# Kernel optimization log

Hardware: AMD Instinct MI355X
Metric: run time of the kernel (lower is better)

The kernel has to match this reference:

```python
import math
import jax, jax.numpy as jnp
from jax import lax
import numpy as np

SQRT2 = 1.4142135623730951
LR_MLP = 0.01


def _blur_kernel():
    k = jnp.array([1., 3., 3., 1.], dtype=jnp.float32)
    k = k[:, None] * k[None, :]
    return k / jnp.sum(k)


def upfirdn2d(x, kernel, up, pad0, pad1):
    # x: (B,C,H,W). Matches torch upfirdn2d_native (flip kernel, zero-upsample, pad, correlate).
    B, C, H, W = x.shape
    x = x.reshape(B * C, 1, H, W)
    k = jnp.flip(kernel, (0, 1))[None, None]
    p1 = pad1 + (up - 1)  # lax lhs_dilation omits trailing zeros of upfirdn upsampling
    out = lax.conv_general_dilated(x, k, (1, 1), ((pad0, p1), (pad0, p1)), lhs_dilation=(up, up))
    return out.reshape(B, C, out.shape[-2], out.shape[-1])


def pixel_norm(x, eps=1e-6):
    norm = jnp.sqrt(jnp.sum(x * x, axis=1, keepdims=True))
    norm = norm / math.sqrt(x.shape[1])
    return x / (norm + eps)


def fused_act(x, b):
    return jax.nn.leaky_relu(x + b[None, :, None, None], 0.2) * SQRT2


def mod_conv(x, w, sw, sb, lat, demodulate, up):
    # w: (Cout,Cin,kh,kw); sw: (Cin, style_ch) equalized-lr linear; lat: (B, style_ch)
    Cout, Cin, kh, kw = w.shape
    s = lat @ (sw.T * (1.0 / math.sqrt(sw.shape[1]))) + sb  # (B, Cin), bias_init=1
    wm = (w * (1.0 / math.sqrt(Cin * kh * kw)))[None] * s[:, None, :, None, None]
    if demodulate:
        d = lax.rsqrt(jnp.sum(wm * wm, axis=(2, 3, 4)) + 1e-8)
        wm = wm * d[:, :, None, None, None]
    if up:
        # per-sample conv_transpose(stride=2, pad=0) == dilated conv with flipped kernel
        def f(xi, wi):
            return lax.conv_general_dilated(xi[None], jnp.flip(wi, (2, 3)), (1, 1),
                                            ((kh - 1, kh - 1), (kw - 1, kw - 1)),
                                            lhs_dilation=(2, 2))[0]
        out = jax.vmap(f)(x, wm)
        out = upfirdn2d(out, _blur_kernel() * 4.0, 1, 1, 1)  # Blur pad=(1,1), k*factor^2
    else:
        pad = kh // 2
        def f(xi, wi):
            return lax.conv_general_dilated(xi[None], wi, (1, 1), ((pad, pad), (pad, pad)))[0]
        out = jax.vmap(f)(x, wm)
    return out


def style_mapping(z, W, Bv):
    x = pixel_norm(z)
    sc = 1.0 / math.sqrt(W.shape[-1])
    for i in range(W.shape[0]):
        x = jax.nn.leaky_relu(x @ (W[i].T * sc) + Bv[i] * LR_MLP, 0.2) * SQRT2
    return x


def setup_inputs() -> dict:
    key = jax.random.key(0)
    ks = jax.random.split(key, 32)
    B = 32
    inp = {
        'z': jax.random.normal(ks[0], (B, 512), jnp.float32),
        'mlp_w': jax.random.normal(ks[1], (8, 512, 512), jnp.float32),
        'mlp_b': jax.random.normal(ks[2], (8, 512), jnp.float32),
        'const_input': jax.random.normal(ks[3], (1, 512, 4, 4), jnp.float32),
        'conv_w': jax.random.normal(ks[4], (9, 512, 512, 3, 3), jnp.float32),
        'conv_style_w': jax.random.normal(ks[5], (9, 512, 512), jnp.float32),
        'conv_style_b': jnp.ones((9, 512), jnp.float32),
        'noise_w': jax.random.normal(ks[6], (9,), jnp.float32),
        'act_bias': jnp.zeros((9, 512), jnp.float32),
        'torgb_w': jax.random.normal(ks[7], (5, 3, 512, 1, 1), jnp.float32),
        'torgb_style_w': jax.random.normal(ks[8], (5, 512, 512), jnp.float32),
        'torgb_style_b': jnp.ones((5, 512), jnp.float32),
        'torgb_bias': jnp.zeros((5, 3), jnp.float32),
    }
    sizes = [4, 8, 8, 16, 16, 32, 32, 64, 64]
    for i, s in enumerate(sizes):
        inp[f'noise{i}'] = jax.random.normal(ks[10 + i], (B, 1, s, s), jnp.float32)
    return inp


def reference(z, mlp_w, mlp_b, const_input, conv_w, conv_style_w, conv_style_b,
              noise_w, act_bias, torgb_w, torgb_style_w, torgb_style_b, torgb_bias,
              noise0, noise1, noise2, noise3, noise4, noise5, noise6, noise7, noise8):
    noises = [noise0, noise1, noise2, noise3, noise4, noise5, noise6, noise7, noise8]
    w = style_mapping(z, mlp_w, mlp_b)  # single style injection -> same w for all layers
    B = z.shape[0]
    x = jnp.tile(const_input, (B, 1, 1, 1))

    def sconv(x, i, up):
        out = mod_conv(x, conv_w[i], conv_style_w[i], conv_style_b[i], w, True, up)
        out = out + noise_w[i] * noises[i]
        return fused_act(out, act_bias[i])

    def trgb(x, j):
        out = mod_conv(x, torgb_w[j], torgb_style_w[j], torgb_style_b[j], w, False, False)
        return out + torgb_bias[j][None, :, None, None]

    x = sconv(x, 0, False)
    skip = trgb(x, 0)
    bk = _blur_kernel() * 4.0
    for r in range(4):  # resolutions 8,16,32,64
        x = sconv(x, 1 + 2 * r, True)
        x = sconv(x, 2 + 2 * r, False)
        skip = trgb(x, r + 1) + upfirdn2d(skip, bk, 2, 2, 1)  # UpsampleUpFIRDn pad=(2,1)
    return skip  # (B,3,64,64)
```

## Files before the change

kernel.cpp:

```cpp
#include <hip/hip_runtime.h>
#include <hip/hip_bf16.h>
#include <cstdio>
#include <math.h>


static constexpr int NB = 32;
static constexpr float SQRT2F      = 1.41421356237309515f;
static constexpr float INV_SQRT512 = 0.04419417382415922f;
static constexpr float INV_SQRT4608= 0.014731391274719742f;

typedef __hip_bfloat16 bf16;
typedef __attribute__((ext_vector_type(8))) short bf16x8;
typedef __attribute__((ext_vector_type(4))) float f32x4;

#define GLOAD_LDS16(src, dst) __builtin_amdgcn_global_load_lds( \
    (const __attribute__((address_space(1))) void*)(src), \
    (__attribute__((address_space(3))) void*)(dst), 16, 0, 0)

__device__ __forceinline__ float lrelu_s2(float v){ return (v > 0.f ? v : 0.2f*v) * SQRT2F; }
__device__ __forceinline__ float bf_lo(unsigned u){ unsigned v = u << 16; return __builtin_bit_cast(float, v); }
__device__ __forceinline__ float bf_hi(unsigned u){ unsigned v = u & 0xffff0000u; return __builtin_bit_cast(float, v); }
__device__ __forceinline__ unsigned packbf2(float a, float b){
  bf16 ha = __float2bfloat16(a), hb = __float2bfloat16(b);
  unsigned short ra = __builtin_bit_cast(unsigned short, ha);
  unsigned short rb = __builtin_bit_cast(unsigned short, hb);
  return (unsigned)ra | ((unsigned)rb << 16);
}

__global__ void k_mapping(const float* __restrict__ z, const float* __restrict__ mlp_w,
                          const float* __restrict__ mlp_b, float* __restrict__ wlat){
  __shared__ float xb[512], yb[512], red[256];
  int b = blockIdx.x, t = threadIdx.x;
  float z0 = z[b*512 + t], z1 = z[b*512 + t + 256];
  red[t] = z0*z0 + z1*z1;
  __syncthreads();
  for(int s = 128; s > 0; s >>= 1){ if(t < s) red[t] += red[t+s]; __syncthreads(); }
  float norm = sqrtf(red[0]) * INV_SQRT512;
  float inv = 1.f / (norm + 1e-6f);
  xb[t] = z0*inv; xb[t+256] = z1*inv;
  __syncthreads();
  for(int l = 0; l < 8; l++){
    const float* Wl = mlp_w + (size_t)l*512*512;
    const float* bl = mlp_b + l*512;
    for(int oo = 0; oo < 2; oo++){
      int o = t + oo*256;
      const float4* wr = (const float4*)(Wl + (size_t)o*512);
      float acc = 0.f;
      #pragma unroll 4
      for(int k = 0; k < 128; k++){
        float4 w4 = wr[k];
        acc += w4.x*xb[4*k] + w4.y*xb[4*k+1] + w4.z*xb[4*k+2] + w4.w*xb[4*k+3];
      }
      yb[o] = lrelu_s2(acc*INV_SQRT512 + bl[o]*0.01f);
    }
    __syncthreads();
    xb[t] = yb[t]; xb[t+256] = yb[t+256];
    __syncthreads();
  }
  wlat[b*512+t] = xb[t]; wlat[b*512+t+256] = xb[t+256];
}

__global__ void k_styles(const float* __restrict__ wlat,
                         const float* __restrict__ csw, const float* __restrict__ csb,
                         const float* __restrict__ tsw, const float* __restrict__ tsb,
                         float* __restrict__ s_conv, float* __restrict__ s_trgb){
  int gid = blockIdx.x*256 + threadIdx.x;
  int l = gid >> 14;
  int b = (gid >> 9) & 31;
  int i = gid & 511;
  const float* row; float bias, wsc;
  if(l < 9){ row = csw + ((size_t)l*512 + i)*512; bias = csb[l*512+i]; wsc = INV_SQRT4608; }
  else     { int lt = l-9; row = tsw + ((size_t)lt*512 + i)*512; bias = tsb[lt*512+i]; wsc = INV_SQRT512; }
  const float4* r4 = (const float4*)row;
  const float4* w4 = (const float4*)(wlat + b*512);
  float acc = 0.f;
  #pragma unroll 4
  for(int k = 0; k < 128; k++){
    float4 a = w4[k], c = r4[k];
    acc += a.x*c.x + a.y*c.y + a.z*c.z + a.w*c.w;
  }
  float s = (acc*INV_SQRT512 + bias) * wsc;
  if(l < 9) s_conv[((size_t)l*32 + b)*512 + i] = s;
  else      s_trgb[((size_t)(l-9)*32 + b)*512 + i] = s;
}

__global__ void k_prep(const float* __restrict__ cw, float* __restrict__ wsq,
                       bf16* __restrict__ wB){
  int gid = blockIdx.x*256 + threadIdx.x;
  const float* p = cw + (size_t)gid*9;
  int l = gid >> 18;
  int oi = gid & 0x3ffff;
  float v[9]; float a = 0.f;
  #pragma unroll
  for(int t = 0; t < 9; t++){ v[t] = p[t]; a += v[t]*v[t]; }
  wsq[gid] = a;
  #pragma unroll
  for(int tap = 0; tap < 9; tap++)
    wB[((size_t)(l*9 + tap) << 18) + oi] = __float2bfloat16(v[tap]);
}

__global__ void k_demod(const float* __restrict__ s_conv, const float* __restrict__ wsq,
                        float* __restrict__ d_conv){
  __shared__ float s2[512];
  int l = blockIdx.x/32, b = blockIdx.x%32, t = threadIdx.x;
  size_t base = ((size_t)l*32 + b)*512;
  float v0 = s_conv[base + t], v1 = s_conv[base + t + 256];
  s2[t] = v0*v0; s2[t+256] = v1*v1;
  __syncthreads();
  for(int oo = 0; oo < 2; oo++){
    int o = t + oo*256;
    const float4* wr = (const float4*)(wsq + ((size_t)l*512 + o)*512);
    float acc = 0.f;
    #pragma unroll 4
    for(int k = 0; k < 128; k++){
      float4 w = wr[k];
      acc += w.x*s2[4*k] + w.y*s2[4*k+1] + w.z*s2[4*k+2] + w.w*s2[4*k+3];
    }
    d_conv[base + o] = rsqrtf(acc + 1e-8f);
  }
}

__global__ void k_ratio(const float* __restrict__ s_conv, const float* __restrict__ s_trgb,
                        float* __restrict__ rat){
  int gid = blockIdx.x*256 + threadIdx.x;
  int lt = gid >> 14;
  if(lt >= 4){ rat[gid] = 1.0f; return; }
  int b = (gid >> 9) & 31;
  int i = gid & 511;
  int cl = 1 + 2*lt;
  float st = s_trgb[((size_t)lt*32 + b)*512 + i];
  float sc = s_conv[((size_t)cl*32 + b)*512 + i];
  rat[gid] = (sc != 0.f) ? st/sc : 0.f;
}

__global__ void k_init(const float* __restrict__ ci, const float* __restrict__ s_conv,
                       bf16* __restrict__ act){
  int gid = blockIdx.x*256 + threadIdx.x;
  int c = gid & 511; int px = (gid >> 9) & 15; int b = gid >> 13;
  act[gid] = __float2bfloat16(ci[c*16 + px] * s_conv[b*512 + c]);
}

template<bool UP>
__global__ __launch_bounds__(256, 2)
void k_conv(const bf16* __restrict__ act, const bf16* __restrict__ wL,
            const float* __restrict__ dL, const float* __restrict__ noise,
            const float* __restrict__ nw_ptr, const float* __restrict__ ab,
            const float* __restrict__ sN, bf16* __restrict__ outp,
            const bf16* __restrict__ zp, int Hin, int Mblocks){
  const int q8 = gridDim.x >> 3;
  const int swzb = (blockIdx.x & 7)*q8 + (blockIdx.x >> 3);
  const int nb = swzb & 3, mb = swzb >> 2;
  if(mb >= Mblocks) return;
  const int mbase = mb*128, nbase = nb*128;

  int py = 0, px = 0;
  int OHy, OHx;
  if(UP){
    int cls = blockIdx.z; py = cls >> 1; px = cls & 1;
    OHy = Hin + 1 - py; OHx = Hin + 1 - px;
  } else {
    OHy = Hin; OHx = Hin;
  }
  const int pixN = OHy*OHx;
  const int Mtot = NB*pixN;
  if(mbase >= Mtot) return;

  __shared__ short As[2][128*64];
  __shared__ short Bs[2][128*64];
  const int t = threadIdx.x;
  const int wid  = t >> 6;
  const int lane = t & 63;
  const int rloc = lane >> 3;
  const int slot = lane & 7;

  int swz[4]; int gbv[4], gYv[4], gXv[4]; bool mv[4];
  const bf16* bB[4];
  #pragma unroll
  for(int i = 0; i < 4; i++){
    int r = wid*32 + i*8 + rloc;
    swz[i] = slot ^ (r & 7);
    int m = mbase + r; mv[i] = (m < Mtot); int mm = mv[i] ? m : 0;
    gbv[i] = mm / pixN; int rem = mm % pixN; gYv[i] = rem / OHx; gXv[i] = rem % OHx;
    bB[i] = wL + ((size_t)(nbase + r) << 9) + swz[i]*8;
  }

  const int mrow0 = (wid >> 1)*64;
  const int ncol0 = (wid & 1)*64;
  const int lr = t & 15;
  const int ks = (t & 63) >> 4;
  const int lr7 = lr & 7;
  const int sw0 = (ks ^ lr7)*8;
  const int sw1 = ((4 + ks) ^ lr7)*8;

  f32x4 acc[4][4];
  #pragma unroll
  for(int i = 0; i < 4; i++)
    #pragma unroll
    for(int j = 0; j < 4; j++) acc[i][j] = (f32x4){0.f,0.f,0.f,0.f};

  int dyl[3], dxl[3], ndy, ndx;
  if(UP){
    if(py == 0){ dyl[0]=0; dyl[1]=2; ndy=2; } else { dyl[0]=1; ndy=1; }
    if(px == 0){ dxl[0]=0; dxl[1]=2; ndx=2; } else { dxl[0]=1; ndx=1; }
  } else {
    dyl[0]=0; dyl[1]=1; dyl[2]=2; ndy=3;
    dxl[0]=0; dxl[1]=1; dxl[2]=2; ndx=3;
  }
  const int TT = ndy*ndx;

  auto mkA = [&](int dy, int dx, const bf16** aA){
    #pragma unroll
    for(int i = 0; i < 4; i++){
      int yy, xx;
      if(UP){ yy = gYv[i] - ((dy - py) >> 1); xx = gXv[i] - ((dx - px) >> 1); }
      else  { yy = gYv[i] + dy - 1;           xx = gXv[i] + dx - 1; }
      bool ok = mv[i] && ((unsigned)yy < (unsigned)Hin) && ((unsigned)xx < (unsigned)Hin);
      aA[i] = ok ? (act + (((size_t)((gbv[i]*Hin + yy)*Hin + xx)) << 9) + swz[i]*8) : zp;
    }
  };
  auto issue = [&](const bf16** aA, int tapIdx, int c, int bb){
    #pragma unroll
    for(int i = 0; i < 4; i++)
      GLOAD_LDS16(aA[i] + c*64, &As[bb][(wid*32 + i*8)*64]);
    #pragma unroll
    for(int i = 0; i < 4; i++)
      GLOAD_LDS16(bB[i] + ((size_t)tapIdx << 18) + c*64, &Bs[bb][(wid*32 + i*8)*64]);
  };

  const bf16* aC[4]; const bf16* aN[4];
  int tapC = dyl[0]*3 + dxl[0], tapN = 0;
  mkA(dyl[0], dxl[0], aC);
  issue(aC, tapC, 0, 0);

  for(int tt = 0; tt < TT; tt++){
    const bool haveNextTap = (tt + 1 < TT);
    if(haveNextTap){
      int dyN = dyl[(tt+1)/ndx], dxN = dxl[(tt+1)%ndx];
      tapN = dyN*3 + dxN;
      mkA(dyN, dxN, aN);
    }
    #pragma unroll
    for(int c = 0; c < 8; c++){
      const int bb = c & 1;
      bool issued = true;
      if(c < 7)               issue(aC, tapC, c+1, bb^1);
      else if(haveNextTap)    issue(aN, tapN, 0,   bb^1);
      else                    issued = false;
      if(issued) asm volatile("s_waitcnt vmcnt(8)" ::: "memory");
      else       asm volatile("s_waitcnt vmcnt(0)" ::: "memory");
      __builtin_amdgcn_s_barrier();
      #pragma unroll
      for(int h = 0; h < 2; h++){
        const int swr = h ? sw1 : sw0;
        bf16x8 af[4], bfr[4];
        #pragma unroll
        for(int f = 0; f < 4; f++){
          af[f]  = *(const bf16x8*)&As[bb][(mrow0 + f*16 + lr)*64 + swr];
          bfr[f] = *(const bf16x8*)&Bs[bb][(ncol0 + f*16 + lr)*64 + swr];
        }
        __builtin_amdgcn_s_setprio(1);
        #pragma unroll
        for(int mf = 0; mf < 4; mf++)
          #pragma unroll
          for(int nf = 0; nf < 4; nf++)
            acc[mf][nf] = __builtin_amdgcn_mfma_f32_16x16x32_bf16(af[mf], bfr[nf], acc[mf][nf], 0, 0, 0);
        __builtin_amdgcn_s_setprio(0);
      }
      asm volatile("s_waitcnt lgkmcnt(0)" ::: "memory");
      __builtin_amdgcn_s_barrier();
    }
    if(haveNextTap){
      #pragma unroll
      for(int i = 0; i < 4; i++) aC[i] = aN[i];
      tapC = tapN;
    }
  }

  const float nwv = UP ? 0.f : *nw_ptr;
  const int U = 2*Hin + 1;
  #pragma unroll
  for(int mf = 0; mf < 4; mf++){
    #pragma unroll
    for(int r = 0; r < 4; r++){
      int me = mbase + mrow0 + mf*16 + ks*4 + r;
      if(me >= Mtot) continue;
      int b = me / pixN; int rem2 = me % pixN; int y = rem2 / OHx, x = rem2 % OHx;
      const float* drow = dL + b*512;
      bf16* orow;
      float nz = 0.f; const float* srow = nullptr;
      if(UP){
        orow = outp + (((size_t)((b*U + 2*y + py))*U + (2*x + px)) << 9);
      } else {
        nz = nwv * noise[(b*OHy + y)*OHx + x];
        srow = sN + b*512;
        orow = outp + ((size_t)me << 9);
      }
      #pragma unroll
      for(int nf = 0; nf < 4; nf++){
        int n = nbase + ncol0 + nf*16 + lr;
        float val = acc[mf][nf][r] * drow[n];
        if(!UP) val = lrelu_s2(val + nz + ab[n]) * srow[n];
        orow[n] = __float2bfloat16(val);
      }
    }
  }
}

__global__ void k_blurF(const bf16* __restrict__ u, const float* __restrict__ noise,
                        const float* __restrict__ nw_ptr, const float* __restrict__ ab,
                        const float* __restrict__ sN, bf16* __restrict__ act, int O){
  const int U = O + 1;
  __shared__ unsigned vrow[65*64];
  const int bid = blockIdx.x;
  const int cq = bid & 3;
  const int rowid = bid >> 2;
  const int Y = rowid % O; const int b = rowid / O;
  const int t = threadIdx.x;
  const int ch2 = t & 63;
  const int cg  = t >> 6;
  const float k1[4] = {0.25f, 0.75f, 0.75f, 0.25f};

  for(int it = 0; it < (65 + 3)/4; it++){
    int col = it*4 + cg;
    if(col < U){
      float a0 = 0.f, a1 = 0.f;
      #pragma unroll
      for(int ky = 0; ky < 4; ky++){
        int yy = Y + ky - 1; if(yy < 0 || yy >= U) continue;
        unsigned uv = *(const unsigned*)(u + (((size_t)(b*U + yy)*U + col) << 9) + cq*128 + ch2*2);
        a0 += k1[ky]*bf_lo(uv); a1 += k1[ky]*bf_hi(uv);
      }
      vrow[col*64 + ch2] = packbf2(a0, a1);
    }
  }
  __syncthreads();
  const float nwv = *nw_ptr;
  const float abA = ab[cq*128 + ch2*2], abB = ab[cq*128 + ch2*2 + 1];
  const float sA  = sN[b*512 + cq*128 + ch2*2], sB = sN[b*512 + cq*128 + ch2*2 + 1];
  for(int it = 0; it < (64 + 3)/4; it++){
    int X = it*4 + cg;
    if(X < O){
      float a0 = 0.f, a1 = 0.f;
      #pragma unroll
      for(int kx = 0; kx < 4; kx++){
        int xx = X + kx - 1; if(xx < 0 || xx >= U) continue;
        unsigned v = vrow[xx*64 + ch2];
        a0 += k1[kx]*bf_lo(v); a1 += k1[kx]*bf_hi(v);
      }
      float nz = nwv * noise[(b*O + Y)*O + X];
      unsigned pk = packbf2(lrelu_s2(a0 + nz + abA)*sA, lrelu_s2(a1 + nz + abB)*sB);
      *(unsigned*)(act + (((size_t)(b*O + Y)*O + X) << 9) + cq*128 + ch2*2) = pk;
    }
  }
}

__global__ void k_torgb(const bf16* __restrict__ act, const float* __restrict__ tw,
                        const float* __restrict__ ratL, const float* __restrict__ tbias,
                        float* __restrict__ dst, int H, int lt, int addflag){
  int wid = threadIdx.x >> 6, lane = threadIdx.x & 63;
  int pix = blockIdx.x*4 + wid;
  int npix = NB*H*H;
  if(pix >= npix) return;
  int b = pix/(H*H);
  const bf16* ap = act + ((size_t)pix << 9);
  const float* rp = ratL + (size_t)b*512;
  const float* w0 = tw + ((size_t)lt*3 + 0)*512;
  const float* w1 = tw + ((size_t)lt*3 + 1)*512;
  const float* w2 = tw + ((size_t)lt*3 + 2)*512;
  float a0 = 0.f, a1 = 0.f, a2 = 0.f;
  #pragma unroll
  for(int j = 0; j < 8; j++){
    int i = lane + j*64;
    float xs = __bfloat162float(ap[i])*rp[i];
    a0 += xs*w0[i]; a1 += xs*w1[i]; a2 += xs*w2[i];
  }
  for(int off = 32; off > 0; off >>= 1){
    a0 += __shfl_xor(a0, off);
    a1 += __shfl_xor(a1, off);
    a2 += __shfl_xor(a2, off);
  }
  if(lane == 0){
    int rem = pix % (H*H);
    size_t o0 = ((size_t)(b*3 + 0)*H*H) + rem;
    size_t o1 = ((size_t)(b*3 + 1)*H*H) + rem;
    size_t o2 = ((size_t)(b*3 + 2)*H*H) + rem;
    float b0 = tbias[lt*3+0], b1 = tbias[lt*3+1], b2 = tbias[lt*3+2];
    if(addflag){ dst[o0] += a0 + b0; dst[o1] += a1 + b1; dst[o2] += a2 + b2; }
    else       { dst[o0]  = a0 + b0; dst[o1]  = a1 + b1; dst[o2]  = a2 + b2; }
  }
}

__global__ void k_skipup(const float* __restrict__ sin, float* __restrict__ sout, int h){
  const int O = 2*h;
  int gid = blockIdx.x*256 + threadIdx.x;
  int total = NB*3*O*O;
  if(gid >= total) return;
  int X = gid % O; int Y = (gid/O) % O; int c = (gid/(O*O)) % 3; int b = gid/(3*O*O);
  const float k1[4] = {1.f, 3.f, 3.f, 1.f};
  float acc = 0.f;
  for(int ky = (Y & 1); ky < 4; ky += 2){
    int ty = Y + ky - 2;
    if(ty < 0) continue;
    int y = ty >> 1; if(y >= h) continue;
    for(int kx = (X & 1); kx < 4; kx += 2){
      int tx = X + kx - 2;
      if(tx < 0) continue;
      int x = tx >> 1; if(x >= h) continue;
      acc += k1[ky]*k1[kx]*(1.f/16.f) * sin[((size_t)(b*3 + c)*h + y)*h + x];
    }
  }
  sout[gid] = acc;
}

extern "C" void kernel_launch(void* const* d_in, const int* in_sizes, int n_in,
                              void* d_out, int out_size, void* d_ws, size_t ws_size,
                              hipStream_t stream){
  const float* z     = (const float*)d_in[0];
  const float* mlp_w = (const float*)d_in[1];
  const float* mlp_b = (const float*)d_in[2];
  const float* cinp  = (const float*)d_in[3];
  const float* conv_w= (const float*)d_in[4];
  const float* csw   = (const float*)d_in[5];
  const float* csb   = (const float*)d_in[6];
  const float* nwp   = (const float*)d_in[7];
  const float* abp   = (const float*)d_in[8];
  const float* tw    = (const float*)d_in[9];
  const float* tsw   = (const float*)d_in[10];
  const float* tsb   = (const float*)d_in[11];
  const float* tb    = (const float*)d_in[12];
  const float* noise[9];
  for(int i = 0; i < 9; i++) noise[i] = (const float*)d_in[13 + i];

  const size_t UMAX = (size_t)32*65*65*512;
  char* base = (char*)d_ws;
  size_t off = 0;
  bf16* buf0 = (bf16*)(base + off); off += UMAX*2;
  bf16* buf1 = (bf16*)(base + off); off += UMAX*2;
  bf16* wB   = (bf16*)(base + off); off += (size_t)9*9*512*512*2;
  float* wsq = (float*)(base + off); off += (size_t)9*512*512*4;
  float* wlat= (float*)(base + off); off += (size_t)32*512*4;
  float* sconv=(float*)(base + off); off += (size_t)9*32*512*4;
  float* dconv=(float*)(base + off); off += (size_t)9*32*512*4;
  float* strgb=(float*)(base + off); off += (size_t)5*32*512*4;
  float* rat  =(float*)(base + off); off += (size_t)5*32*512*4;
  float* skipA=(float*)(base + off); off += (size_t)32*3*64*64*4;
  float* skipB=(float*)(base + off); off += (size_t)32*3*64*64*4;
  bf16* zpage=(bf16*)(base + off); off += 2048;
  if(ws_size < off){
    fprintf(stderr, "kernel_launch: ws too small (%zu < %zu)\n", ws_size, off);
    return;
  }
  float* out = (float*)d_out;

  hipMemsetAsync(zpage, 0, 2048, stream);
  k_mapping<<<32, 256, 0, stream>>>(z, mlp_w, mlp_b, wlat);
  k_styles <<<896, 256, 0, stream>>>(wlat, csw, csb, tsw, tsb, sconv, strgb);
  k_prep   <<<9216, 256, 0, stream>>>(conv_w, wsq, wB);
  k_demod  <<<288, 256, 0, stream>>>(sconv, wsq, dconv);
  k_ratio  <<<320, 256, 0, stream>>>(sconv, strgb, rat);
  k_init   <<<1024, 256, 0, stream>>>(cinp, sconv, buf0);

  auto conv_noup = [&](const bf16* in, bf16* o, int H, int layer, const float* sN){
    int M = 32*H*H; int Mb = (M + 127)/128;
    int Gx = ((Mb*4 + 7)/8)*8;
    k_conv<false><<<dim3(Gx,1,1), 256, 0, stream>>>(in, wB + ((size_t)layer*9 << 18),
        dconv + (size_t)layer*NB*512, noise[layer], nwp + layer, abp + layer*512, sN, o, zpage, H, Mb);
  };
  auto conv_up = [&](const bf16* in, bf16* o, int Hin, int layer){
    int Mmax = 32*(Hin+1)*(Hin+1); int Mb = (Mmax + 127)/128;
    int Gx = ((Mb*4 + 7)/8)*8;
    k_conv<true><<<dim3(Gx,1,4), 256, 0, stream>>>(in, wB + ((size_t)layer*9 << 18),
        dconv + (size_t)layer*NB*512, nullptr, nullptr, nullptr, nullptr, o, zpage, Hin, Mb);
  };
  auto blur = [&](const bf16* u, bf16* o, int O, int layer, const float* sN){
    int blocks = 32*O*4;
    k_blurF<<<blocks, 256, 0, stream>>>(u, noise[layer], nwp + layer,
        abp + layer*512, sN, o, O);
  };
  auto torgb = [&](const bf16* act, float* dst, int H, int lt, int add){
    int npix = 32*H*H;
    k_torgb<<<(npix + 3)/4, 256, 0, stream>>>(act, tw, rat + (size_t)lt*NB*512, tb, dst, H, lt, add);
  };
  auto skipup = [&](const float* sin, float* sout, int h){
    int total = 32*3*(2*h)*(2*h);
    k_skipup<<<(total + 255)/256, 256, 0, stream>>>(sin, sout, h);
  };

  const float* S = sconv;
  const float* sT4 = strgb + (size_t)4*NB*512;

  conv_noup(buf0, buf1, 4, 0, S + (size_t)1*NB*512);
  torgb(buf1, skipA, 4, 0, 0);

  conv_up(buf1, buf0, 4, 1);
  blur(buf0, buf1, 8, 1, S + (size_t)2*NB*512);
  conv_noup(buf1, buf0, 8, 2, S + (size_t)3*NB*512);
  skipup(skipA, skipB, 4);
  torgb(buf0, skipB, 8, 1, 1);

  conv_up(buf0, buf1, 8, 3);
  blur(buf1, buf0, 16, 3, S + (size_t)4*NB*512);
  conv_noup(buf0, buf1, 16, 4, S + (size_t)5*NB*512);
  skipup(skipB, skipA, 8);
  torgb(buf1, skipA, 16, 2, 1);

  conv_up(buf1, buf0, 16, 5);
  blur(buf0, buf1, 32, 5, S + (size_t)6*NB*512);
  conv_noup(buf1, buf0, 32, 6, S + (size_t)7*NB*512);
  skipup(skipA, skipB, 16);
  torgb(buf0, skipB, 32, 3, 1);

  conv_up(buf0, buf1, 32, 7);
  blur(buf1, buf0, 64, 7, S + (size_t)8*NB*512);
  conv_noup(buf0, buf1, 64, 8, sT4);
  skipup(skipB, out, 32);
  torgb(buf1, out, 64, 4, 1);
}
```

Baseline: 2.106 ms.

## Add 256x256-tile conv kernel with 512 threads for larger non-upsampling layers

Adds a new implicit-GEMM conv kernel (k_conv2) that uses 256x256 output tiles, 8 waves per block and an 8x4 MFMA fragment grid per wave. It is used for non-upsampling convolutions at resolution 16 and above. The larger tiles raise arithmetic intensity and reuse of each staged A/B tile, at the cost of 128KB LDS, one block per CU and more accumulator registers. It also removes the s_setprio bracketing around the MFMA loop in the existing kernel.

New measurement: 2.242 ms. +6.5%, slower.

```diff
diff --git a/kernel.cpp b/kernel.cpp
--- a/kernel.cpp
+++ b/kernel.cpp
@@ -258,13 +258,11 @@
           af[f]  = *(const bf16x8*)&As[bb][(mrow0 + f*16 + lr)*64 + swr];
           bfr[f] = *(const bf16x8*)&Bs[bb][(ncol0 + f*16 + lr)*64 + swr];
         }
-        __builtin_amdgcn_s_setprio(1);
         #pragma unroll
         for(int mf = 0; mf < 4; mf++)
           #pragma unroll
           for(int nf = 0; nf < 4; nf++)
             acc[mf][nf] = __builtin_amdgcn_mfma_f32_16x16x32_bf16(af[mf], bfr[nf], acc[mf][nf], 0, 0, 0);
-        __builtin_amdgcn_s_setprio(0);
       }
       asm volatile("s_waitcnt lgkmcnt(0)" ::: "memory");
       __builtin_amdgcn_s_barrier();
@@ -300,6 +298,142 @@
         int n = nbase + ncol0 + nf*16 + lr;
         float val = acc[mf][nf][r] * drow[n];
         if(!UP) val = lrelu_s2(val + nz + ab[n]) * srow[n];
+        orow[n] = __float2bfloat16(val);
+      }
+    }
+  }
+}
+
+__global__ __launch_bounds__(512, 1)
+void k_conv2(const bf16* __restrict__ act, const bf16* __restrict__ wL,
+             const float* __restrict__ dL, const float* __restrict__ noise,
+             const float* __restrict__ nw_ptr, const float* __restrict__ ab,
+             const float* __restrict__ sN, bf16* __restrict__ outp,
+             const bf16* __restrict__ zp, int Hin, int Mblocks){
+  const int q8 = gridDim.x >> 3;
+  const int swzb = (blockIdx.x & 7)*q8 + (blockIdx.x >> 3);
+  const int nb = swzb & 1, mb = swzb >> 1;
+  if(mb >= Mblocks) return;
+  const int mbase = mb*256, nbase = nb*256;
+  const int pixN = Hin*Hin;
+  const int Mtot = NB*pixN;
+  if(mbase >= Mtot) return;
+
+  __shared__ short As[2][256*64];
+  __shared__ short Bs[2][256*64];
+  const int t = threadIdx.x;
+  const int wid  = t >> 6;
+  const int lane = t & 63;
+  const int rloc = lane >> 3;
+  const int slot = lane & 7;
+
+  int swz[4]; int gbv[4], gYv[4], gXv[4]; bool mv[4];
+  const bf16* bB[4];
+  #pragma unroll
+  for(int i = 0; i < 4; i++){
+    int r = wid*32 + i*8 + rloc;
+    swz[i] = slot ^ (r & 7);
+    int m = mbase + r; mv[i] = (m < Mtot); int mm = mv[i] ? m : 0;
+    gbv[i] = mm / pixN; int rem = mm % pixN; gYv[i] = rem / Hin; gXv[i] = rem % Hin;
+    bB[i] = wL + ((size_t)(nbase + r) << 9) + swz[i]*8;
+  }
+
+  const int mrow0 = (wid >> 2)*128;
+  const int ncol0 = (wid & 3)*64;
+  const int lr = t & 15;
+  const int ks = (t & 63) >> 4;
+  const int lr7 = lr & 7;
+  const int sw0 = (ks ^ lr7)*8;
+  const int sw1 = ((4 + ks) ^ lr7)*8;
+
+  f32x4 acc[8][4];
+  #pragma unroll
+  for(int i = 0; i < 8; i++)
+    #pragma unroll
+    for(int j = 0; j < 4; j++) acc[i][j] = (f32x4){0.f,0.f,0.f,0.f};
+
+  auto mkA = [&](int dy, int dx, const bf16** aA){
+    #pragma unroll
+    for(int i = 0; i < 4; i++){
+      int yy = gYv[i] + dy - 1, xx = gXv[i] + dx - 1;
+      bool ok = mv[i] && ((unsigned)yy < (unsigned)Hin) && ((unsigned)xx < (unsigned)Hin);
+      aA[i] = ok ? (act + (((size_t)((gbv[i]*Hin + yy)*Hin + xx)) << 9) + swz[i]*8) : zp;
+    }
+  };
+  auto issue = [&](const bf16** aA, int tapIdx, int c, int bb){
+    #pragma unroll
+    for(int i = 0; i < 4; i++)
+      GLOAD_LDS16(aA[i] + c*64, &As[bb][(wid*32 + i*8)*64]);
+    #pragma unroll
+    for(int i = 0; i < 4; i++)
+      GLOAD_LDS16(bB[i] + ((size_t)tapIdx << 18) + c*64, &Bs[bb][(wid*32 + i*8)*64]);
+  };
+
+  const bf16* aC[4]; const bf16* aN[4];
+  int tapC = 0, tapN = 0;
+  mkA(0, 0, aC);
+  issue(aC, 0, 0, 0);
+
+  for(int tt = 0; tt < 9; tt++){
+    const bool haveNextTap = (tt + 1 < 9);
+    if(haveNextTap){
+      int dyN = (tt+1)/3, dxN = (tt+1)%3;
+      tapN = tt + 1;
+      mkA(dyN, dxN, aN);
+    }
+    #pragma unroll
+    for(int c = 0; c < 8; c++){
+      const int bb = c & 1;
+      bool issued = true;
+      if(c < 7)               issue(aC, tapC, c+1, bb^1);
+      else if(haveNextTap)    issue(aN, tapN, 0,   bb^1);
+      else                    issued = false;
+      if(issued) asm volatile("s_waitcnt vmcnt(8)" ::: "memory");
+      else       asm volatile("s_waitcnt vmcnt(0)" ::: "memory");
+      __builtin_amdgcn_s_barrier();
+      #pragma unroll
+      for(int h = 0; h < 2; h++){
+        const int swr = h ? sw1 : sw0;
+        bf16x8 af[8], bfr[4];
+        #pragma unroll
+        for(int f = 0; f < 8; f++)
+          af[f]  = *(const bf16x8*)&As[bb][(mrow0 + f*16 + lr)*64 + swr];
+        #pragma unroll
+        for(int f = 0; f < 4; f++)
+          bfr[f] = *(const bf16x8*)&Bs[bb][(ncol0 + f*16 + lr)*64 + swr];
+        #pragma unroll
+        for(int mf = 0; mf < 8; mf++)
+          #pragma unroll
+          for(int nf = 0; nf < 4; nf++)
+            acc[mf][nf] = __builtin_amdgcn_mfma_f32_16x16x32_bf16(af[mf], bfr[nf], acc[mf][nf], 0, 0, 0);
+      }
+      asm volatile("s_waitcnt lgkmcnt(0)" ::: "memory");
+      __builtin_amdgcn_s_barrier();
+    }
+    if(haveNextTap){
+      #pragma unroll
+      for(int i = 0; i < 4; i++) aC[i] = aN[i];
+      tapC = tapN;
+    }
+  }
+
+  const float nwv = *nw_ptr;
+  #pragma unroll
+  for(int mf = 0; mf < 8; mf++){
+    #pragma unroll
+    for(int r = 0; r < 4; r++){
+      int me = mbase + mrow0 + mf*16 + ks*4 + r;
+      if(me >= Mtot) continue;
+      int b = me / pixN; int rem2 = me % pixN; int y = rem2 / Hin, x = rem2 % Hin;
+      const float* drow = dL + b*512;
+      float nz = nwv * noise[(b*Hin + y)*Hin + x];
+      const float* srow = sN + b*512;
+      bf16* orow = outp + ((size_t)me << 9);
+      #pragma unroll
+      for(int nf = 0; nf < 4; nf++){
+        int n = nbase + ncol0 + nf*16 + lr;
+        float val = acc[mf][nf][r] * drow[n];
+        val = lrelu_s2(val + nz + ab[n]) * srow[n];
         orow[n] = __float2bfloat16(val);
       }
     }
@@ -461,10 +595,17 @@
   k_init   <<<1024, 256, 0, stream>>>(cinp, sconv, buf0);
 
   auto conv_noup = [&](const bf16* in, bf16* o, int H, int layer, const float* sN){
-    int M = 32*H*H; int Mb = (M + 127)/128;
-    int Gx = ((Mb*4 + 7)/8)*8;
-    k_conv<false><<<dim3(Gx,1,1), 256, 0, stream>>>(in, wB + ((size_t)layer*9 << 18),
-        dconv + (size_t)layer*NB*512, noise[layer], nwp + layer, abp + layer*512, sN, o, zpage, H, Mb);
+    if(H >= 16){
+      int M = 32*H*H; int Mb = (M + 255)/256;
+      int Gx = ((Mb*2 + 7)/8)*8;
+      k_conv2<<<dim3(Gx,1,1), 512, 0, stream>>>(in, wB + ((size_t)layer*9 << 18),
+          dconv + (size_t)layer*NB*512, noise[layer], nwp + layer, abp + layer*512, sN, o, zpage, H, Mb);
+    } else {
+      int M = 32*H*H; int Mb = (M + 127)/128;
+      int Gx = ((Mb*4 + 7)/8)*8;
+      k_conv<false><<<dim3(Gx,1,1), 256, 0, stream>>>(in, wB + ((size_t)layer*9 << 18),
+          dconv + (size_t)layer*NB*512, noise[layer], nwp + layer, abp + layer*512, sN, o, zpage, H, Mb);
+    }
   };
   auto conv_up = [&](const bf16* in, bf16* o, int Hin, int layer){
     int Mmax = 32*(Hin+1)*(Hin+1); int Mb = (Mmax + 127)/128;
```
